# Performance work log

Hardware: AMD Instinct MI355X
Metric: run time of the kernel (lower is better)

Reference implementation:

```python
import jax, jax.numpy as jnp
import numpy as np

HIDDEN = 512
HEADS = 8
HEAD_DIM = HIDDEN // HEADS


def setup_inputs() -> dict:
    key = jax.random.key(0)
    ks = jax.random.split(key, 7)
    B, C, H, W = 8, HIDDEN, 32, 32
    scale = 1.0 / np.sqrt(C)
    inputs = jax.random.normal(ks[0], (B, C, H, W), dtype=jnp.float32)
    # 1x1 conv == per-pixel linear; store weights as [C_in, C_out]
    wq = jax.random.normal(ks[1], (C, HIDDEN), dtype=jnp.float32) * scale
    wk = jax.random.normal(ks[2], (C, HIDDEN), dtype=jnp.float32) * scale
    wv = jax.random.normal(ks[3], (C, HIDDEN), dtype=jnp.float32) * scale
    bq = jax.random.normal(ks[4], (HIDDEN,), dtype=jnp.float32) * 0.01
    bk = jax.random.normal(ks[5], (HIDDEN,), dtype=jnp.float32) * 0.01
    bv = jax.random.normal(ks[6], (HIDDEN,), dtype=jnp.float32) * 0.01
    return {"inputs": inputs, "wq": wq, "bq": bq, "wk": wk, "bk": bk, "wv": wv, "bv": bv}


def _proj_heads(x, w, b):
    # x: [B,C,H,W] -> tokens [B,heads,N,head_dim], matching transpose_for_scores
    B, C, H, W = x.shape
    t = jnp.einsum('bchw,cd->bhwd', x, w) + b          # [B,H,W,HIDDEN]
    t = t.reshape(B, H * W, HEADS, HEAD_DIM)
    return t.transpose(0, 2, 1, 3)                      # [B,heads,N,hd]


def reference(inputs, wq, bq, wk, bk, wv, bv):
    B, C, H, W = inputs.shape
    q = _proj_heads(inputs, wq, bq)
    k = _proj_heads(inputs, wk, bk)
    v = _proj_heads(inputs, wv, bv)
    # NOTE: original module applies NO 1/sqrt(d) scaling
    scores = jnp.einsum('bhnd,bhmd->bhnm', q, k)        # [B,heads,N,N]
    probs = jax.nn.softmax(scores, axis=-1)
    ctx = jnp.einsum('bhnm,bhmd->bhnd', probs, v)       # [B,heads,N,hd]
    # [B,heads,N,hd] -> [B,N,heads*hd] -> [B,H,W,C] -> [B,C,H,W]
    out = ctx.transpose(0, 2, 1, 3).reshape(B, H, W, HEADS * HEAD_DIM)
    return out.transpose(0, 3, 1, 2)
```

## Files before the change

kernel.cpp:

```cpp
#include <hip/hip_runtime.h>
#include <hip/hip_bf16.h>
#include <cmath>

#define B_     8
#define C_     512
#define N_     1024
#define HEADS_ 8
#define HD_    64
#define INST_  64

typedef short     v8s __attribute__((ext_vector_type(8)));
typedef _Float16  v8h __attribute__((ext_vector_type(8)));
typedef float    v16f __attribute__((ext_vector_type(16)));
typedef unsigned short ushort_t;
typedef unsigned int   uint_t;

__device__ inline ushort_t f2h(float x) {
    _Float16 h = (_Float16)x;
    ushort_t r; __builtin_memcpy(&r, &h, 2); return r;
}
__device__ inline uint_t pkbf(float a, float b) {
    __hip_bfloat162 p = __float22bfloat162_rn(make_float2(a, b));
    uint_t r; __builtin_memcpy(&r, &p, 4); return r;
}

__global__ __launch_bounds__(256) void prep_kernel(
    const float* __restrict__ wq, const float* __restrict__ wk,
    const float* __restrict__ wv,
    uint_t* __restrict__ wt)
{
    __shared__ uint_t LH[64 * 32];
    const int z = blockIdx.z;
    const float* src = (z == 0) ? wq : (z == 1) ? wk : wv;
    const size_t outRow0 = (size_t)z * 512 + blockIdx.x * 64;

    const int d0 = blockIdx.x * 64;
    const int c0 = blockIdx.y * 64;
    const int t  = threadIdx.x;

    #pragma unroll
    for (int rep = 0; rep < 2; ++rep) {
        int idx = rep * 256 + t;
        int cp  = idx >> 4;
        int dq  = idx & 15;
        float4 fa = *(const float4*)&src[(size_t)(c0 + 2 * cp) * 512 + d0 + dq * 4];
        float4 fb = *(const float4*)&src[(size_t)(c0 + 2 * cp + 1) * 512 + d0 + dq * 4];
        float aa[4] = {fa.x, fa.y, fa.z, fa.w};
        float bb[4] = {fb.x, fb.y, fb.z, fb.w};
        #pragma unroll
        for (int j = 0; j < 4; ++j) {
            int d_l = dq * 4 + j;
            LH[d_l * 32 + (cp ^ (d_l & 31))] =
                (uint_t)f2h(aa[j]) | ((uint_t)f2h(bb[j]) << 16);
        }
    }
    __syncthreads();

    const int d_l = t >> 2;
    const int wq4 = (t & 3) * 8;
    uint_t vh[8];
    #pragma unroll
    for (int i = 0; i < 8; ++i)
        vh[i] = LH[d_l * 32 + ((wq4 + i) ^ (d_l & 31))];
    size_t base = (outRow0 + d_l) * 256 + c0 / 2 + wq4;
    *(uint4*)&((uint_t*)wt)[base]     = *(uint4*)&vh[0];
    *(uint4*)&((uint_t*)wt)[base + 4] = *(uint4*)&vh[4];
}

__global__ __launch_bounds__(256) void proj_kernel(
    const float* __restrict__ x, const _Float16* __restrict__ wt,
    const float* __restrict__ bq, const float* __restrict__ bk,
    const float* __restrict__ bv,
    ushort_t* __restrict__ qf, ushort_t* __restrict__ kf,
    ushort_t* __restrict__ vt)
{
    __shared__ _Float16 POOL[8192];
    _Float16* As = POOL;
    _Float16* Bs = POOL + 2048;
    uint_t*   Asu = (uint_t*)POOL;

    const int tok0  = blockIdx.x * 64;
    const int b     = tok0 >> 10;
    const int ntb   = tok0 & 1023;
    const int by    = blockIdx.y;
    const int which = by >> 2;
    const int nloc0 = (by & 3) * 128;

    const int t   = threadIdx.x;
    const int w   = t >> 6;
    const int l   = t & 63;
    const int l31 = l & 31;
    const int h5  = l >> 5;
    const int wm  = w & 1;
    const int wn  = w >> 1;

    const int g   = t & 3;
    const int r0  = t >> 2;
    const int swz = g ^ (r0 & 3);
    const _Float16* baseB = wt + (size_t)(which * 512 + nloc0 + r0) * 512 + g * 8;

    const int cp = t & 15;
    const int tq = t >> 4;
    const float* baseX = x + (size_t)b * 524288 + (size_t)(2 * cp) * 1024
                       + ntb + 4 * tq;

    float4 pfa0, pfa1; v8h pfb0, pfb1;
    auto load_tile = [&](int s) {
        pfa0 = *(const float4*)(baseX + (size_t)s * 32768);
        pfa1 = *(const float4*)(baseX + (size_t)s * 32768 + 1024);
        pfb0 = *(const v8h*)(baseB + s * 32);
        pfb1 = *(const v8h*)(baseB + 32768 + s * 32);
    };
    auto store_tile = [&]() {
        float a0[4] = {pfa0.x, pfa0.y, pfa0.z, pfa0.w};
        float a1[4] = {pfa1.x, pfa1.y, pfa1.z, pfa1.w};
        #pragma unroll
        for (int i = 0; i < 4; ++i) {
            int rm = 4 * tq + i;
            Asu[rm * 16 + ((cp >> 2) ^ i) * 4 + (cp & 3)] =
                (uint_t)f2h(a0[i]) | ((uint_t)f2h(a1[i]) << 16);
        }
        *(v8h*)&Bs[(r0 * 4 + swz) * 8] = pfb0;
        int row = 64 + r0;
        *(v8h*)&Bs[(row * 4 + (g ^ (row & 3))) * 8] = pfb1;
    };

    v16f acc[2] = {{}, {}};

    load_tile(0);
    store_tile();
    __syncthreads();

    for (int step = 0; step < 16; ++step) {
        if (step < 15) load_tile(step + 1);

        #pragma unroll
        for (int kc = 0; kc < 2; ++kc) {
            int rm = wm * 32 + l31;
            v8h af = *(const v8h*)&As[(rm * 4 + ((kc * 2 + h5) ^ (rm & 3))) * 8];
            v8h bf[2];
            #pragma unroll
            for (int ns = 0; ns < 2; ++ns) {
                int rn = wn * 64 + ns * 32 + l31;
                bf[ns] = *(const v8h*)&Bs[(rn * 4 + ((kc * 2 + h5) ^ (rn & 3))) * 8];
            }
            #pragma unroll
            for (int ns = 0; ns < 2; ++ns)
                acc[ns] = __builtin_amdgcn_mfma_f32_32x32x16_f16(
                    af, bf[ns], acc[ns], 0, 0, 0);
        }

        __syncthreads();
        if (step < 15) {
            store_tile();
            __syncthreads();
        }
    }

    if (which < 2) {
        ushort_t* oh = (which == 0) ? qf : kf;
        const float* bias = (which == 0) ? bq : bk;
        #pragma unroll
        for (int ns = 0; ns < 2; ++ns) {
            int d_local = nloc0 + wn * 64 + ns * 32 + l31;
            float bvv  = bias[d_local];
            int head   = d_local >> 6;
            int hd     = d_local & 63;
            size_t pb  = (size_t)(b * HEADS_ + head) * 65536 + hd;
            #pragma unroll
            for (int r = 0; r < 16; ++r) {
                int n = ntb + wm * 32 + (r & 3) + 8 * (r >> 2) + 4 * h5;
                oh[pb + (size_t)n * 64] = f2h(acc[ns][r] + bvv);
            }
        }
    } else {
        float bvv[2];
        #pragma unroll
        for (int ns = 0; ns < 2; ++ns)
            bvv[ns] = bv[nloc0 + wn * 64 + ns * 32 + l31];
        __syncthreads();
        uint_t* TW = (uint_t*)POOL + w * 1024;
        #pragma unroll
        for (int ns = 0; ns < 2; ++ns)
            #pragma unroll
            for (int r = 0; r < 16; r += 2) {
                int tok_l = (r & 3) + 8 * (r >> 2) + 4 * h5;
                int hd_l  = ns * 32 + l31;
                TW[hd_l * 16 + ((tok_l >> 1) ^ (hd_l & 15))] =
                    pkbf(acc[ns][r] + bvv[ns], acc[ns][r + 1] + bvv[ns]);
            }
        __syncthreads();
        const int head = (nloc0 + wn * 64) >> 6;
        uint_t* vtu = (uint_t*)vt;
        size_t base = (size_t)(b * HEADS_ + head) * 32768 + (size_t)l * 512
                    + (ntb + wm * 32) / 2;
        #pragma unroll
        for (int c = 0; c < 4; ++c) {
            uint_t wd[4];
            #pragma unroll
            for (int kk = 0; kk < 4; ++kk) {
                int wsx = c * 4 + kk;
                int w3 = wsx & 7;
                int sw = (wsx & ~7) | (w3 & 1) | (((w3 >> 1) & 1) << 2)
                                   | (((w3 >> 2) & 1) << 1);
                wd[kk] = TW[l * 16 + (sw ^ (l & 15))];
            }
            *(uint4*)&vtu[base + c * 4] = *(uint4*)&wd[0];
        }
    }
}

__global__ __launch_bounds__(256) void attn_kernel(
    const ushort_t* __restrict__ qf, const ushort_t* __restrict__ kf,
    const ushort_t* __restrict__ vt, float* __restrict__ out)
{
    __shared__ _Float16 KH[4096];
    __shared__ ushort_t VT[4096];
    __shared__ float    RS[128];

    const int inst  = blockIdx.x;
    const int chunk = blockIdx.y;
    const int t     = threadIdx.x;
    const int w     = t >> 6;
    const int l     = t & 63;
    const int l31   = l & 31;
    const int h5    = l >> 5;

    const ushort_t* Qf = qf + (size_t)inst * 65536;
    const ushort_t* Kf = kf + (size_t)inst * 65536;
    const ushort_t* Vt = vt + (size_t)inst * 65536;

    const int qbase = chunk * 128 + w * 32;

    v8h aq[4];
    #pragma unroll
    for (int ks = 0; ks < 4; ++ks)
        aq[ks] = *(const v8h*)&Qf[(size_t)(qbase + l31) * 64 + ks * 16 + h5 * 8];

    const int g   = t & 7;
    const int r0  = t >> 3;
    const int swz = g ^ (r0 & 7);
    const ushort_t* baseK = Kf + (size_t)r0 * 64 + g * 8;
    const ushort_t* baseV = Vt + (size_t)r0 * 1024 + g * 8;

    v8h pk0, pk1; v8s pv0, pv1;
    auto load_tile = [&](int kt) {
        pk0 = *(const v8h*)(baseK + (size_t)kt * 4096);
        pk1 = *(const v8h*)(baseK + (size_t)kt * 4096 + 2048);
        pv0 = *(const v8s*)(baseV + (size_t)kt * 64);
        pv1 = *(const v8s*)(baseV + 32768 + (size_t)kt * 64);
    };
    auto store_tile = [&]() {
        int so0 = (r0 * 8 + swz) * 8;
        int so1 = ((32 + r0) * 8 + swz) * 8;
        *(v8h*)&KH[so0] = pk0;
        *(v8h*)&KH[so1] = pk1;
        *(v8s*)&VT[so0] = pv0;
        *(v8s*)&VT[so1] = pv1;
    };

    v16f O0 = {}, O1 = {};
    float rsumv = 0.f;

    load_tile(0);
    store_tile();
    __syncthreads();

    for (int kt = 0; kt < 16; ++kt) {
        if (kt < 15) load_tile(kt + 1);

        #pragma unroll
        for (int t2 = 0; t2 < 2; ++t2) {
            v16f s = {};
            int kvrow = t2 * 32 + l31;
            __builtin_amdgcn_s_setprio(1);
            #pragma unroll
            for (int ks = 0; ks < 4; ++ks) {
                int so = (kvrow * 8 + ((ks * 2 + h5) ^ (kvrow & 7))) * 8;
                v8h khf = *(const v8h*)&KH[so];
                s = __builtin_amdgcn_mfma_f32_32x32x16_f16(khf, aq[ks], s, 0, 0, 0);
            }
            __builtin_amdgcn_s_setprio(0);
            float e0[8], e1[8];
            #pragma unroll
            for (int j = 0; j < 8; ++j) {
                e0[j] = __expf(s[j] - 64.0f);
                e1[j] = __expf(s[8 + j] - 64.0f);
                rsumv += e0[j] + e1[j];
            }
            uint4 u0, u1;
            u0.x = pkbf(e0[0], e0[1]); u0.y = pkbf(e0[2], e0[3]);
            u0.z = pkbf(e0[4], e0[5]); u0.w = pkbf(e0[6], e0[7]);
            u1.x = pkbf(e1[0], e1[1]); u1.y = pkbf(e1[2], e1[3]);
            u1.z = pkbf(e1[4], e1[5]); u1.w = pkbf(e1[6], e1[7]);
            v8s p0 = __builtin_bit_cast(v8s, u0);
            v8s p1 = __builtin_bit_cast(v8s, u1);

            __builtin_amdgcn_s_setprio(1);
            #pragma unroll
            for (int hh = 0; hh < 2; ++hh) {
                int rv = hh * 32 + l31;
                int g0 = (4 * t2 + h5)     ^ (rv & 7);
                int g1 = (4 * t2 + 2 + h5) ^ (rv & 7);
                v8s bv0 = *(const v8s*)&VT[(rv * 8 + g0) * 8];
                v8s bv1 = *(const v8s*)&VT[(rv * 8 + g1) * 8];
                if (hh == 0) {
                    O0 = __builtin_amdgcn_mfma_f32_32x32x16_bf16(p0, bv0, O0, 0, 0, 0);
                    O0 = __builtin_amdgcn_mfma_f32_32x32x16_bf16(p1, bv1, O0, 0, 0, 0);
                } else {
                    O1 = __builtin_amdgcn_mfma_f32_32x32x16_bf16(p0, bv0, O1, 0, 0, 0);
                    O1 = __builtin_amdgcn_mfma_f32_32x32x16_bf16(p1, bv1, O1, 0, 0, 0);
                }
            }
            __builtin_amdgcn_s_setprio(0);
        }

        __syncthreads();
        if (kt < 15) {
            store_tile();
            __syncthreads();
        }
    }

    float tot = rsumv + __shfl_xor(rsumv, 32, 64);
    if (h5 == 0) RS[w * 32 + l31] = 1.0f / tot;
    __syncthreads();
    float invr[16];
    #pragma unroll
    for (int r = 0; r < 16; ++r)
        invr[r] = RS[w * 32 + (r & 3) + 8 * (r >> 2) + 4 * h5];

    const int b    = inst >> 3;
    const int head = inst & 7;
    float* ob = out + (size_t)b * C_ * N_;
    #pragma unroll
    for (int hh = 0; hh < 2; ++hh) {
        const v16f& O = hh ? O1 : O0;
        int c = head * 64 + hh * 32 + l31;
        #pragma unroll
        for (int qd = 0; qd < 4; ++qd) {
            int n = qbase + 8 * qd + 4 * h5;
            float4 o4;
            o4.x = O[qd * 4 + 0] * invr[qd * 4 + 0];
            o4.y = O[qd * 4 + 1] * invr[qd * 4 + 1];
            o4.z = O[qd * 4 + 2] * invr[qd * 4 + 2];
            o4.w = O[qd * 4 + 3] * invr[qd * 4 + 3];
            *(float4*)&ob[(size_t)c * N_ + n] = o4;
        }
    }
}

extern "C" void kernel_launch(void* const* d_in, const int* in_sizes, int n_in,
                              void* d_out, int out_size, void* d_ws, size_t ws_size,
                              hipStream_t stream) {
    const float* x  = (const float*)d_in[0];
    const float* wq = (const float*)d_in[1];
    const float* bq = (const float*)d_in[2];
    const float* wk = (const float*)d_in[3];
    const float* bk = (const float*)d_in[4];
    const float* wv = (const float*)d_in[5];
    const float* bv = (const float*)d_in[6];
    float* out = (float*)d_out;

    char* ws = (char*)d_ws;
    _Float16* wt = (_Float16*)(ws);
    ushort_t* qf = (ushort_t*)(ws + 9961472);
    ushort_t* kf = (ushort_t*)(ws + 18350080);
    ushort_t* vt = (ushort_t*)(ws + 26738688);

    prep_kernel<<<dim3(8, 8, 3), 256, 0, stream>>>(wq, wk, wv, (uint_t*)wt);
    proj_kernel<<<dim3(128, 12), 256, 0, stream>>>(x, wt, bq, bk, bv,
                                                   qf, kf, vt);
    attn_kernel<<<dim3(64, 8), 256, 0, stream>>>(qf, kf, vt, out);
}
```

Before: 147.9 us.

## Enlarge proj GEMM tile to 128 tokens with double-buffered LDS

The projection kernel now computes 128 tokens per block instead of 64, giving each warp a 2x2 grid of MFMA tiles so every loaded A/B fragment is reused twice. LDS is double-buffered, which drops one barrier per k-step, and the swizzle is changed to suit the wider tile. The grid is halved and launch bounds request 3 blocks per CU. Separately, the setprio hints in the attention kernel are removed. Costs are more accumulator registers and fewer blocks (768) to spread across the CUs.

```diff
diff --git a/kernel.cpp b/kernel.cpp
--- a/kernel.cpp
+++ b/kernel.cpp
@@ -67,19 +67,16 @@
     *(uint4*)&((uint_t*)wt)[base + 4] = *(uint4*)&vh[4];
 }
 
-__global__ __launch_bounds__(256) void proj_kernel(
+__global__ __launch_bounds__(256, 3) void proj_kernel(
     const float* __restrict__ x, const _Float16* __restrict__ wt,
     const float* __restrict__ bq, const float* __restrict__ bk,
     const float* __restrict__ bv,
     ushort_t* __restrict__ qf, ushort_t* __restrict__ kf,
     ushort_t* __restrict__ vt)
 {
-    __shared__ _Float16 POOL[8192];
-    _Float16* As = POOL;
-    _Float16* Bs = POOL + 2048;
-    uint_t*   Asu = (uint_t*)POOL;
-
-    const int tok0  = blockIdx.x * 64;
+    __shared__ _Float16 POOL[16384];
+
+    const int tok0  = blockIdx.x * 128;
     const int b     = tok0 >> 10;
     const int ntb   = tok0 & 1023;
     const int by    = blockIdx.y;
@@ -96,63 +93,80 @@
 
     const int g   = t & 3;
     const int r0  = t >> 2;
-    const int swz = g ^ (r0 & 3);
+    const int sr0 = (r0 & 3) ^ ((r0 >> 2) & 3);
     const _Float16* baseB = wt + (size_t)(which * 512 + nloc0 + r0) * 512 + g * 8;
 
     const int cp = t & 15;
     const int tq = t >> 4;
     const float* baseX = x + (size_t)b * 524288 + (size_t)(2 * cp) * 1024
-                       + ntb + 4 * tq;
-
-    float4 pfa0, pfa1; v8h pfb0, pfb1;
+                       + ntb + 8 * tq;
+
+    float4 pa00, pa01, pa10, pa11; v8h pfb0, pfb1;
     auto load_tile = [&](int s) {
-        pfa0 = *(const float4*)(baseX + (size_t)s * 32768);
-        pfa1 = *(const float4*)(baseX + (size_t)s * 32768 + 1024);
+        const float* px = baseX + (size_t)s * 32768;
+        pa00 = *(const float4*)(px);
+        pa01 = *(const float4*)(px + 4);
+        pa10 = *(const float4*)(px + 1024);
+        pa11 = *(const float4*)(px + 1028);
         pfb0 = *(const v8h*)(baseB + s * 32);
         pfb1 = *(const v8h*)(baseB + 32768 + s * 32);
     };
-    auto store_tile = [&]() {
-        float a0[4] = {pfa0.x, pfa0.y, pfa0.z, pfa0.w};
-        float a1[4] = {pfa1.x, pfa1.y, pfa1.z, pfa1.w};
-        #pragma unroll
-        for (int i = 0; i < 4; ++i) {
-            int rm = 4 * tq + i;
-            Asu[rm * 16 + ((cp >> 2) ^ i) * 4 + (cp & 3)] =
+    auto store_tile = [&](int off) {
+        uint_t* Asu = (uint_t*)(POOL + off);
+        float a0[8] = {pa00.x, pa00.y, pa00.z, pa00.w,
+                       pa01.x, pa01.y, pa01.z, pa01.w};
+        float a1[8] = {pa10.x, pa10.y, pa10.z, pa10.w,
+                       pa11.x, pa11.y, pa11.z, pa11.w};
+        #pragma unroll
+        for (int i = 0; i < 8; ++i) {
+            int rm  = 8 * tq + i;
+            int srm = (rm & 3) ^ ((rm >> 2) & 3);
+            Asu[rm * 16 + ((cp >> 2) ^ srm) * 4 + (cp & 3)] =
                 (uint_t)f2h(a0[i]) | ((uint_t)f2h(a1[i]) << 16);
         }
-        *(v8h*)&Bs[(r0 * 4 + swz) * 8] = pfb0;
-        int row = 64 + r0;
-        *(v8h*)&Bs[(row * 4 + (g ^ (row & 3))) * 8] = pfb1;
+        _Float16* Bs = POOL + off + 4096;
+        *(v8h*)&Bs[(r0 * 4 + (g ^ sr0)) * 8] = pfb0;
+        *(v8h*)&Bs[((64 + r0) * 4 + (g ^ sr0)) * 8] = pfb1;
     };
 
-    v16f acc[2] = {{}, {}};
+    v16f acc[2][2] = {{{}, {}}, {{}, {}}};
 
     load_tile(0);
-    store_tile();
+    store_tile(0);
     __syncthreads();
 
     for (int step = 0; step < 16; ++step) {
+        const int off  = (step & 1) ? 8192 : 0;
+        const int offn = (step & 1) ? 0 : 8192;
         if (step < 15) load_tile(step + 1);
 
         #pragma unroll
         for (int kc = 0; kc < 2; ++kc) {
-            int rm = wm * 32 + l31;
-            v8h af = *(const v8h*)&As[(rm * 4 + ((kc * 2 + h5) ^ (rm & 3))) * 8];
-            v8h bf[2];
-            #pragma unroll
-            for (int ns = 0; ns < 2; ++ns) {
-                int rn = wn * 64 + ns * 32 + l31;
-                bf[ns] = *(const v8h*)&Bs[(rn * 4 + ((kc * 2 + h5) ^ (rn & 3))) * 8];
-            }
-            #pragma unroll
-            for (int ns = 0; ns < 2; ++ns)
-                acc[ns] = __builtin_amdgcn_mfma_f32_32x32x16_f16(
-                    af, bf[ns], acc[ns], 0, 0, 0);
-        }
-
-        __syncthreads();
+            v8h af[2], bf[2];
+            #pragma unroll
+            for (int mi = 0; mi < 2; ++mi) {
+                int rm  = wm * 64 + mi * 32 + l31;
+                int srm = (rm & 3) ^ ((rm >> 2) & 3);
+                af[mi] = *(const v8h*)&POOL[off +
+                           (rm * 4 + ((kc * 2 + h5) ^ srm)) * 8];
+            }
+            #pragma unroll
+            for (int ni = 0; ni < 2; ++ni) {
+                int rn  = wn * 64 + ni * 32 + l31;
+                int srn = (rn & 3) ^ ((rn >> 2) & 3);
+                bf[ni] = *(const v8h*)&POOL[off + 4096 +
+                           (rn * 4 + ((kc * 2 + h5) ^ srn)) * 8];
+            }
+            #pragma unroll
+            for (int mi = 0; mi < 2; ++mi)
+                #pragma unroll
+                for (int ni = 0; ni < 2; ++ni)
+                    acc[mi][ni] = __builtin_amdgcn_mfma_f32_32x32x16_f16(
+                        af[mi], bf[ni], acc[mi][ni], 0, 0, 0);
+        }
+
         if (step < 15) {
-            store_tile();
+            store_tile(offn);
             __syncthreads();
         }
     }
@@ -161,41 +175,47 @@
         ushort_t* oh = (which == 0) ? qf : kf;
         const float* bias = (which == 0) ? bq : bk;
         #pragma unroll
-        for (int ns = 0; ns < 2; ++ns) {
-            int d_local = nloc0 + wn * 64 + ns * 32 + l31;
+        for (int ni = 0; ni < 2; ++ni) {
+            int d_local = nloc0 + wn * 64 + ni * 32 + l31;
             float bvv  = bias[d_local];
             int head   = d_local >> 6;
             int hd     = d_local & 63;
             size_t pb  = (size_t)(b * HEADS_ + head) * 65536 + hd;
             #pragma unroll
-            for (int r = 0; r < 16; ++r) {
-                int n = ntb + wm * 32 + (r & 3) + 8 * (r >> 2) + 4 * h5;
-                oh[pb + (size_t)n * 64] = f2h(acc[ns][r] + bvv);
-            }
+            for (int mi = 0; mi < 2; ++mi)
+                #pragma unroll
+                for (int r = 0; r < 16; ++r) {
+                    int n = ntb + wm * 64 + mi * 32
+                          + (r & 3) + 8 * (r >> 2) + 4 * h5;
+                    oh[pb + (size_t)n * 64] = f2h(acc[mi][ni][r] + bvv);
+                }
         }
     } else {
         float bvv[2];
         #pragma unroll
-        for (int ns = 0; ns < 2; ++ns)
-            bvv[ns] = bv[nloc0 + wn * 64 + ns * 32 + l31];
+        for (int ni = 0; ni < 2; ++ni)
+            bvv[ni] = bv[nloc0 + wn * 64 + ni * 32 + l31];
         __syncthreads();
-        uint_t* TW = (uint_t*)POOL + w * 1024;
-        #pragma unroll
-        for (int ns = 0; ns < 2; ++ns)
-            #pragma unroll
-            for (int r = 0; r < 16; r += 2) {
-                int tok_l = (r & 3) + 8 * (r >> 2) + 4 * h5;
-                int hd_l  = ns * 32 + l31;
-                TW[hd_l * 16 + ((tok_l >> 1) ^ (hd_l & 15))] =
-                    pkbf(acc[ns][r] + bvv[ns], acc[ns][r + 1] + bvv[ns]);
-            }
+        uint_t* TW = (uint_t*)POOL + w * 2048;
+        #pragma unroll
+        for (int mi = 0; mi < 2; ++mi)
+            #pragma unroll
+            for (int ni = 0; ni < 2; ++ni)
+                #pragma unroll
+                for (int r = 0; r < 16; r += 2) {
+                    int tok_l = mi * 32 + (r & 3) + 8 * (r >> 2) + 4 * h5;
+                    int hd_l  = ni * 32 + l31;
+                    TW[hd_l * 32 + ((tok_l >> 1) ^ (hd_l & 31))] =
+                        pkbf(acc[mi][ni][r] + bvv[ni],
+                             acc[mi][ni][r + 1] + bvv[ni]);
+                }
         __syncthreads();
         const int head = (nloc0 + wn * 64) >> 6;
         uint_t* vtu = (uint_t*)vt;
         size_t base = (size_t)(b * HEADS_ + head) * 32768 + (size_t)l * 512
-                    + (ntb + wm * 32) / 2;
-        #pragma unroll
-        for (int c = 0; c < 4; ++c) {
+                    + (ntb + wm * 64) / 2;
+        #pragma unroll
+        for (int c = 0; c < 8; ++c) {
             uint_t wd[4];
             #pragma unroll
             for (int kk = 0; kk < 4; ++kk) {
@@ -203,7 +223,7 @@
                 int w3 = wsx & 7;
                 int sw = (wsx & ~7) | (w3 & 1) | (((w3 >> 1) & 1) << 2)
                                    | (((w3 >> 2) & 1) << 1);
-                wd[kk] = TW[l * 16 + (sw ^ (l & 15))];
+                wd[kk] = TW[l * 32 + (sw ^ (l & 31))];
             }
             *(uint4*)&vtu[base + c * 4] = *(uint4*)&wd[0];
         }
@@ -273,14 +293,12 @@
         for (int t2 = 0; t2 < 2; ++t2) {
             v16f s = {};
             int kvrow = t2 * 32 + l31;
-            __builtin_amdgcn_s_setprio(1);
             #pragma unroll
             for (int ks = 0; ks < 4; ++ks) {
                 int so = (kvrow * 8 + ((ks * 2 + h5) ^ (kvrow & 7))) * 8;
                 v8h khf = *(const v8h*)&KH[so];
                 s = __builtin_amdgcn_mfma_f32_32x32x16_f16(khf, aq[ks], s, 0, 0, 0);
             }
-            __builtin_amdgcn_s_setprio(0);
             float e0[8], e1[8];
             #pragma unroll
             for (int j = 0; j < 8; ++j) {
@@ -296,7 +314,6 @@
             v8s p0 = __builtin_bit_cast(v8s, u0);
             v8s p1 = __builtin_bit_cast(v8s, u1);
 
-            __builtin_amdgcn_s_setprio(1);
             #pragma unroll
             for (int hh = 0; hh < 2; ++hh) {
                 int rv = hh * 32 + l31;
@@ -312,7 +329,6 @@
                     O1 = __builtin_amdgcn_mfma_f32_32x32x16_bf16(p1, bv1, O1, 0, 0, 0);
                 }
             }
-            __builtin_amdgcn_s_setprio(0);
         }
 
         __syncthreads();
@@ -369,7 +385,7 @@
     ushort_t* vt = (ushort_t*)(ws + 26738688);
 
     prep_kernel<<<dim3(8, 8, 3), 256, 0, stream>>>(wq, wk, wv, (uint_t*)wt);
-    proj_kernel<<<dim3(128, 12), 256, 0, stream>>>(x, wt, bq, bk, bv,
-                                                   qf, kf, vt);
+    proj_kernel<<<dim3(64, 12), 256, 0, stream>>>(x, wt, bq, bk, bv,
+                                                  qf, kf, vt);
     attn_kernel<<<dim3(64, 8), 256, 0, stream>>>(qf, kf, vt, out);
 }
```

New measurement: 149.1 us. About the same (+0.8%).

## Double-buffer LDS tiles with two-deep register prefetch in projection and attention

Applied to the files above, without the earlier changes.

Both kernels now keep two LDS tile buffers and alternate even and odd register prefetch sets. The next tile is written into the idle buffer while the current one is computed, which drops one barrier per K step and hides global load latency further. The projection kernel also switches to a two-level XOR swizzle to cut LDS bank conflicts, and the attention kernel drops its s_setprio hints. The cost is more LDS per block and more registers, which may lower occupancy.

```diff
diff --git a/kernel.cpp b/kernel.cpp
--- a/kernel.cpp
+++ b/kernel.cpp
@@ -74,10 +74,7 @@
     ushort_t* __restrict__ qf, ushort_t* __restrict__ kf,
     ushort_t* __restrict__ vt)
 {
-    __shared__ _Float16 POOL[8192];
-    _Float16* As = POOL;
-    _Float16* Bs = POOL + 2048;
-    uint_t*   Asu = (uint_t*)POOL;
+    __shared__ _Float16 POOL[12288];
 
     const int tok0  = blockIdx.x * 64;
     const int b     = tok0 >> 10;
@@ -96,7 +93,7 @@
 
     const int g   = t & 3;
     const int r0  = t >> 2;
-    const int swz = g ^ (r0 & 3);
+    const int sr0 = (r0 & 3) ^ ((r0 >> 2) & 3);
     const _Float16* baseB = wt + (size_t)(which * 512 + nloc0 + r0) * 512 + g * 8;
 
     const int cp = t & 15;
@@ -104,55 +101,92 @@
     const float* baseX = x + (size_t)b * 524288 + (size_t)(2 * cp) * 1024
                        + ntb + 4 * tq;
 
-    float4 pfa0, pfa1; v8h pfb0, pfb1;
-    auto load_tile = [&](int s) {
-        pfa0 = *(const float4*)(baseX + (size_t)s * 32768);
-        pfa1 = *(const float4*)(baseX + (size_t)s * 32768 + 1024);
-        pfb0 = *(const v8h*)(baseB + s * 32);
-        pfb1 = *(const v8h*)(baseB + 32768 + s * 32);
-    };
-    auto store_tile = [&]() {
-        float a0[4] = {pfa0.x, pfa0.y, pfa0.z, pfa0.w};
-        float a1[4] = {pfa1.x, pfa1.y, pfa1.z, pfa1.w};
+    float4 paE0, paE1, paO0, paO1;
+    v8h    pbE0, pbE1, pbO0, pbO1;
+
+    auto loadE = [&](int s) {
+        const float* px = baseX + (size_t)s * 32768;
+        paE0 = *(const float4*)(px);
+        paE1 = *(const float4*)(px + 1024);
+        pbE0 = *(const v8h*)(baseB + s * 32);
+        pbE1 = *(const v8h*)(baseB + 32768 + s * 32);
+    };
+    auto loadO = [&](int s) {
+        const float* px = baseX + (size_t)s * 32768;
+        paO0 = *(const float4*)(px);
+        paO1 = *(const float4*)(px + 1024);
+        pbO0 = *(const v8h*)(baseB + s * 32);
+        pbO1 = *(const v8h*)(baseB + 32768 + s * 32);
+    };
+    auto storeE = [&](int off) {
+        uint_t* Asu = (uint_t*)(POOL + off);
+        float a0[4] = {paE0.x, paE0.y, paE0.z, paE0.w};
+        float a1[4] = {paE1.x, paE1.y, paE1.z, paE1.w};
         #pragma unroll
         for (int i = 0; i < 4; ++i) {
-            int rm = 4 * tq + i;
-            Asu[rm * 16 + ((cp >> 2) ^ i) * 4 + (cp & 3)] =
+            int rm  = 4 * tq + i;
+            int srm = i ^ (tq & 3);
+            Asu[rm * 16 + ((cp >> 2) ^ srm) * 4 + (cp & 3)] =
                 (uint_t)f2h(a0[i]) | ((uint_t)f2h(a1[i]) << 16);
         }
-        *(v8h*)&Bs[(r0 * 4 + swz) * 8] = pfb0;
-        int row = 64 + r0;
-        *(v8h*)&Bs[(row * 4 + (g ^ (row & 3))) * 8] = pfb1;
+        _Float16* Bs = POOL + off + 2048;
+        *(v8h*)&Bs[(r0 * 4 + (g ^ sr0)) * 8] = pbE0;
+        *(v8h*)&Bs[((64 + r0) * 4 + (g ^ sr0)) * 8] = pbE1;
+    };
+    auto storeO = [&](int off) {
+        uint_t* Asu = (uint_t*)(POOL + off);
+        float a0[4] = {paO0.x, paO0.y, paO0.z, paO0.w};
+        float a1[4] = {paO1.x, paO1.y, paO1.z, paO1.w};
+        #pragma unroll
+        for (int i = 0; i < 4; ++i) {
+            int rm  = 4 * tq + i;
+            int srm = i ^ (tq & 3);
+            Asu[rm * 16 + ((cp >> 2) ^ srm) * 4 + (cp & 3)] =
+                (uint_t)f2h(a0[i]) | ((uint_t)f2h(a1[i]) << 16);
+        }
+        _Float16* Bs = POOL + off + 2048;
+        *(v8h*)&Bs[(r0 * 4 + (g ^ sr0)) * 8] = pbO0;
+        *(v8h*)&Bs[((64 + r0) * 4 + (g ^ sr0)) * 8] = pbO1;
     };
 
     v16f acc[2] = {{}, {}};
 
-    load_tile(0);
-    store_tile();
-    __syncthreads();
-
-    for (int step = 0; step < 16; ++step) {
-        if (step < 15) load_tile(step + 1);
-
+    auto compute = [&](int off) {
         #pragma unroll
         for (int kc = 0; kc < 2; ++kc) {
-            int rm = wm * 32 + l31;
-            v8h af = *(const v8h*)&As[(rm * 4 + ((kc * 2 + h5) ^ (rm & 3))) * 8];
+            int rm  = wm * 32 + l31;
+            int srm = (rm & 3) ^ ((rm >> 2) & 3);
+            v8h af = *(const v8h*)&POOL[off + (rm * 4 + ((kc * 2 + h5) ^ srm)) * 8];
             v8h bf[2];
             #pragma unroll
             for (int ns = 0; ns < 2; ++ns) {
-                int rn = wn * 64 + ns * 32 + l31;
-                bf[ns] = *(const v8h*)&Bs[(rn * 4 + ((kc * 2 + h5) ^ (rn & 3))) * 8];
+                int rn  = wn * 64 + ns * 32 + l31;
+                int srn = (rn & 3) ^ ((rn >> 2) & 3);
+                bf[ns] = *(const v8h*)&POOL[off + 2048 +
+                           (rn * 4 + ((kc * 2 + h5) ^ srn)) * 8];
             }
             #pragma unroll
             for (int ns = 0; ns < 2; ++ns)
                 acc[ns] = __builtin_amdgcn_mfma_f32_32x32x16_f16(
                     af, bf[ns], acc[ns], 0, 0, 0);
         }
-
+    };
+
+    loadE(0);
+    loadO(1);
+    storeE(0);
+    __syncthreads();
+
+    for (int sp = 0; sp < 8; ++sp) {
+        const int s = 2 * sp;
+        if (s < 14) loadE(s + 2);
+        compute(0);
+        storeO(6144);
         __syncthreads();
-        if (step < 15) {
-            store_tile();
+        if (s < 13) loadO(s + 3);
+        compute(6144);
+        if (s < 14) {
+            storeE(0);
             __syncthreads();
         }
     }
@@ -214,8 +248,8 @@
     const ushort_t* __restrict__ qf, const ushort_t* __restrict__ kf,
     const ushort_t* __restrict__ vt, float* __restrict__ out)
 {
-    __shared__ _Float16 KH[4096];
-    __shared__ ushort_t VT[4096];
+    __shared__ _Float16 KH[8192];
+    __shared__ ushort_t VT[8192];
     __shared__ float    RS[128];
 
     const int inst  = blockIdx.x;
@@ -243,44 +277,52 @@
     const ushort_t* baseK = Kf + (size_t)r0 * 64 + g * 8;
     const ushort_t* baseV = Vt + (size_t)r0 * 1024 + g * 8;
 
-    v8h pk0, pk1; v8s pv0, pv1;
-    auto load_tile = [&](int kt) {
-        pk0 = *(const v8h*)(baseK + (size_t)kt * 4096);
-        pk1 = *(const v8h*)(baseK + (size_t)kt * 4096 + 2048);
-        pv0 = *(const v8s*)(baseV + (size_t)kt * 64);
-        pv1 = *(const v8s*)(baseV + 32768 + (size_t)kt * 64);
-    };
-    auto store_tile = [&]() {
+    v8h pkE0, pkE1, pkO0, pkO1;
+    v8s pvE0, pvE1, pvO0, pvO1;
+
+    auto loadE = [&](int kt) {
+        pkE0 = *(const v8h*)(baseK + (size_t)kt * 4096);
+        pkE1 = *(const v8h*)(baseK + (size_t)kt * 4096 + 2048);
+        pvE0 = *(const v8s*)(baseV + (size_t)kt * 64);
+        pvE1 = *(const v8s*)(baseV + 32768 + (size_t)kt * 64);
+    };
+    auto loadO = [&](int kt) {
+        pkO0 = *(const v8h*)(baseK + (size_t)kt * 4096);
+        pkO1 = *(const v8h*)(baseK + (size_t)kt * 4096 + 2048);
+        pvO0 = *(const v8s*)(baseV + (size_t)kt * 64);
+        pvO1 = *(const v8s*)(baseV + 32768 + (size_t)kt * 64);
+    };
+    auto storeE = [&](int off) {
         int so0 = (r0 * 8 + swz) * 8;
         int so1 = ((32 + r0) * 8 + swz) * 8;
-        *(v8h*)&KH[so0] = pk0;
-        *(v8h*)&KH[so1] = pk1;
-        *(v8s*)&VT[so0] = pv0;
-        *(v8s*)&VT[so1] = pv1;
+        *(v8h*)&KH[off + so0] = pkE0;
+        *(v8h*)&KH[off + so1] = pkE1;
+        *(v8s*)&VT[off + so0] = pvE0;
+        *(v8s*)&VT[off + so1] = pvE1;
+    };
+    auto storeO = [&](int off) {
+        int so0 = (r0 * 8 + swz) * 8;
+        int so1 = ((32 + r0) * 8 + swz) * 8;
+        *(v8h*)&KH[off + so0] = pkO0;
+        *(v8h*)&KH[off + so1] = pkO1;
+        *(v8s*)&VT[off + so0] = pvO0;
+        *(v8s*)&VT[off + so1] = pvO1;
     };
 
     v16f O0 = {}, O1 = {};
     float rsumv = 0.f;
 
-    load_tile(0);
-    store_tile();
-    __syncthreads();
-
-    for (int kt = 0; kt < 16; ++kt) {
-        if (kt < 15) load_tile(kt + 1);
-
+    auto compute = [&](int off) {
         #pragma unroll
         for (int t2 = 0; t2 < 2; ++t2) {
             v16f s = {};
             int kvrow = t2 * 32 + l31;
-            __builtin_amdgcn_s_setprio(1);
             #pragma unroll
             for (int ks = 0; ks < 4; ++ks) {
                 int so = (kvrow * 8 + ((ks * 2 + h5) ^ (kvrow & 7))) * 8;
-                v8h khf = *(const v8h*)&KH[so];
+                v8h khf = *(const v8h*)&KH[off + so];
                 s = __builtin_amdgcn_mfma_f32_32x32x16_f16(khf, aq[ks], s, 0, 0, 0);
             }
-            __builtin_amdgcn_s_setprio(0);
             float e0[8], e1[8];
             #pragma unroll
             for (int j = 0; j < 8; ++j) {
@@ -296,14 +338,13 @@
             v8s p0 = __builtin_bit_cast(v8s, u0);
             v8s p1 = __builtin_bit_cast(v8s, u1);
 
-            __builtin_amdgcn_s_setprio(1);
             #pragma unroll
             for (int hh = 0; hh < 2; ++hh) {
                 int rv = hh * 32 + l31;
                 int g0 = (4 * t2 + h5)     ^ (rv & 7);
                 int g1 = (4 * t2 + 2 + h5) ^ (rv & 7);
-                v8s bv0 = *(const v8s*)&VT[(rv * 8 + g0) * 8];
-                v8s bv1 = *(const v8s*)&VT[(rv * 8 + g1) * 8];
+                v8s bv0 = *(const v8s*)&VT[off + (rv * 8 + g0) * 8];
+                v8s bv1 = *(const v8s*)&VT[off + (rv * 8 + g1) * 8];
                 if (hh == 0) {
                     O0 = __builtin_amdgcn_mfma_f32_32x32x16_bf16(p0, bv0, O0, 0, 0, 0);
                     O0 = __builtin_amdgcn_mfma_f32_32x32x16_bf16(p1, bv1, O0, 0, 0, 0);
@@ -312,12 +353,24 @@
                     O1 = __builtin_amdgcn_mfma_f32_32x32x16_bf16(p1, bv1, O1, 0, 0, 0);
                 }
             }
-            __builtin_amdgcn_s_setprio(0);
-        }
-
+        }
+    };
+
+    loadE(0);
+    loadO(1);
+    storeE(0);
+    __syncthreads();
+
+    for (int sp = 0; sp < 8; ++sp) {
+        const int kt = 2 * sp;
+        if (kt < 14) loadE(kt + 2);
+        compute(0);
+        storeO(4096);
         __syncthreads();
-        if (kt < 15) {
-            store_tile();
+        if (kt < 13) loadO(kt + 3);
+        compute(4096);
+        if (kt < 14) {
+            storeE(0);
             __syncthreads();
         }
     }
```

New measurement: 141.5 us. -4.3%, faster.
